# Optimization experiments

Hardware: AMD Instinct MI355X
Metric: run time of the kernel (lower is better)

Reference implementation:

```python
import jax, jax.numpy as jnp
import numpy as np

INIT_L = 512.0
EPS = 1e-6
N_HEAD = 16


def fire_bias(T, w1, b1, w2, b2, c, L_multiplier):
    # positions and relative distances
    pos = jnp.arange(T, dtype=jnp.float32)
    rel = pos[:, None] - pos[None, :]                      # (T, T)
    threshold = jnp.abs(L_multiplier * INIT_L)
    pos_norm = jnp.maximum(pos, threshold)[:, None]        # (T, 1)
    rel = jnp.log(jnp.abs(c * rel) + 1.0)                  # (T, T)
    pos_norm = jnp.log(jnp.abs(c * pos_norm) + 1.0) + EPS  # (T, 1)
    nd = rel / pos_norm                                    # (T, T)
    # tiny MLP: 1 -> mlp_width -> n_head
    h = jax.nn.relu(nd[..., None] * w1[0] + b1)            # (T, T, 32)
    bias = jnp.einsum('tsw,wh->hts', h, w2) + b2[:, None, None]  # (H, T, T)
    causal = jnp.tril(jnp.ones((T, T), dtype=bool))
    bias = jnp.where(causal[None], bias, -jnp.inf)
    return bias[None]                                      # (1, H, T, T)


def reference(x, Wqkv, bqkv, Wproj, bproj, w1, b1, w2, b2, c_param, L_multiplier):
    B, T, C = x.shape
    H = N_HEAD
    hd = C // H
    qkv = x @ Wqkv + bqkv                                  # (B, T, 3C)
    q, k, v = jnp.split(qkv, 3, axis=-1)
    q = q.reshape(B, T, H, hd).transpose(0, 2, 1, 3)       # (B, H, T, hd)
    k = k.reshape(B, T, H, hd).transpose(0, 2, 1, 3)
    v = v.reshape(B, T, H, hd).transpose(0, 2, 1, 3)
    bias = fire_bias(T, w1, b1, w2, b2, c_param, L_multiplier)  # (1, H, T, T)
    scale = 1.0 / jnp.sqrt(jnp.float32(hd))
    att = jnp.einsum('bhqd,bhkd->bhqk', q, k) * scale + bias
    att = jax.nn.softmax(att, axis=-1)
    y = jnp.einsum('bhqk,bhkd->bhqd', att, v)              # (B, H, T, hd)
    y = y.transpose(0, 2, 1, 3).reshape(B, T, C)
    return y @ Wproj + bproj


def setup_inputs() -> dict:
    key = jax.random.key(0)
    ks = jax.random.split(key, 8)
    B, T, C, H, W = 2, 2048, 1024, 16, 32
    s = 0.02
    return {
        'x': jax.random.normal(ks[0], (B, T, C), jnp.float32),
        'Wqkv': jax.random.normal(ks[1], (C, 3 * C), jnp.float32) * s,
        'bqkv': jnp.zeros((3 * C,), jnp.float32),
        'Wproj': jax.random.normal(ks[2], (C, C), jnp.float32) * s,
        'bproj': jnp.zeros((C,), jnp.float32),
        'w1': jax.random.normal(ks[3], (1, W), jnp.float32),
        'b1': jnp.zeros((W,), jnp.float32),
        'w2': jax.random.normal(ks[4], (W, H), jnp.float32) * 0.1,
        'b2': jnp.zeros((H,), jnp.float32),
        'c_param': jnp.float32(0.1),
        'L_multiplier': jnp.float32(1.0),
    }
```

## Files before the change

kernel.cpp:

```cpp
#include <hip/hip_runtime.h>
#include <cstdint>

typedef unsigned short u16;
typedef unsigned int u32;

typedef short bf16x8 __attribute__((ext_vector_type(8)));
typedef float f32x4 __attribute__((ext_vector_type(4)));

#define LN2 0.69314718055994530942f
#define LOG2E 1.44269504088896340736f
#define INFF __builtin_inff()

__device__ __forceinline__ u16 f2bf(float f) {
  u32 u = __float_as_uint(f);
  u = (u + 0x7fffu + ((u >> 16) & 1u)) >> 16;
  return (u16)u;
}
__device__ __forceinline__ u32 pack2bf(float a, float b) {
  u32 ta = __float_as_uint(a) + 0x8000u;
  u32 tb = __float_as_uint(b) + 0x8000u;
  return __builtin_amdgcn_perm(tb, ta, 0x07060302u);
}
__device__ __forceinline__ u32 pack2bf_rne(float a, float b) {
  return (u32)f2bf(a) | ((u32)f2bf(b) << 16);
}

#if __has_builtin(__builtin_amdgcn_global_load_lds)
#define HAVE_GLDS 1
__device__ __forceinline__ void glds16(const u16* g, u16* l) {
  __builtin_amdgcn_global_load_lds((const __attribute__((address_space(1))) void*)g,
                                   (__attribute__((address_space(3))) void*)l, 16, 0, 0);
}
#else
#define HAVE_GLDS 0
#endif

__device__ __forceinline__ void stage1k(const u16* gperlane, u16* lwave, int lane) {
#if HAVE_GLDS
  (void)lane;
  glds16(gperlane, lwave);
#else
  *(uint4*)(lwave + lane * 8) = *(const uint4*)gperlane;
#endif
}

__device__ __forceinline__ u16* swzp(u16* base, int row, int bc) {
  return (u16*)((char*)base + row * 128 + (bc ^ ((row & 7) << 4)));
}


__global__ void k_convert_x(const float* __restrict__ in, u16* __restrict__ out, int n4) {
  int i = blockIdx.x * blockDim.x + threadIdx.x;
  if (i < n4) {
    float4 v = ((const float4*)in)[i];
    ushort4 o;
    o.x = f2bf(v.x); o.y = f2bf(v.y); o.z = f2bf(v.z); o.w = f2bf(v.w);
    ((ushort4*)out)[i] = o;
  }
}

__global__ void k_transpose_bf(const float* __restrict__ in, u16* __restrict__ out, int R, int C) {
  __shared__ float t[32][33];
  int c0 = blockIdx.x * 32, r0 = blockIdx.y * 32;
  int tx = threadIdx.x, ty = threadIdx.y;
#pragma unroll
  for (int k = 0; k < 4; k++) t[ty + 8 * k][tx] = in[(size_t)(r0 + ty + 8 * k) * C + c0 + tx];
  __syncthreads();
#pragma unroll
  for (int k = 0; k < 4; k++) out[(size_t)(c0 + ty + 8 * k) * R + r0 + tx] = f2bf(t[tx][ty + 8 * k]);
}

__global__ void k_tables(const float* __restrict__ cP, const float* __restrict__ lP,
                         float* __restrict__ ig2, float* __restrict__ rl) {
  int t = blockIdx.x * blockDim.x + threadIdx.x;
  float c = fabsf(cP[0]);
  if (t < 2048) {
    float lm = lP[0];
    float thr = fabsf(lm * 512.0f);
    float pn = fmaxf((float)t, thr);
    float den = logf(c * pn + 1.0f) + 1e-6f;
    ig2[t] = LN2 / den;
  }
  if (t < 2112) {
    int d = t - 63;
    if (d < 0) d = 0;
    rl[t] = log2f(c * (float)d + 1.0f);
  }
}

__global__ void k_segments(const float* __restrict__ w1, const float* __restrict__ b1,
                           const float* __restrict__ w2, const float* __restrict__ b2,
                           float* __restrict__ segX, float* __restrict__ segA,
                           float* __restrict__ segB, int* __restrict__ segU) {
  __shared__ float xs[32];
  __shared__ float srt[32];
  __shared__ float uniq[32];
  __shared__ int uCnt;
  int t = threadIdx.x;
  if (t < 32) {
    float w = w1[t], b = b1[t];
    xs[t] = (w != 0.0f) ? (-b / w) : INFF;
  }
  __syncthreads();
  if (t < 32) {
    float x = xs[t];
    int r = 0;
    for (int v = 0; v < 32; v++) {
      float xv = xs[v];
      if (xv < x || (xv == x && v < t)) r++;
    }
    srt[r] = x;
  }
  __syncthreads();
  if (t == 0) {
    int u = 0;
    for (int i = 0; i < 32; i++) {
      float v = srt[i];
      if (v < 3.0e38f && (u == 0 || v != uniq[u - 1])) uniq[u++] = v;
    }
    uCnt = u;
    segU[0] = u;
  }
  __syncthreads();
  int u = uCnt;
  if (t < u) segX[t] = uniq[t];
  for (int idx = t; idx < (u + 1) * 16; idx += blockDim.x) {
    int j = idx >> 4, h = idx & 15;
    float p;
    if (u == 0) p = 0.0f;
    else if (j == 0) p = uniq[0] - 1.0f;
    else if (j == u) p = uniq[u - 1] + 1.0f;
    else p = 0.5f * (uniq[j - 1] + uniq[j]);
    float A = b2[h], B = 0.0f;
    for (int w = 0; w < 32; w++) {
      float w1w = w1[w], b1w = b1[w], w2wh = w2[w * 16 + h];
      if (w1w != 0.0f) {
        if (fmaf(w1w, p, b1w) > 0.0f) { B += w1w * w2wh; A += b1w * w2wh; }
      } else if (b1w > 0.0f) {
        A += b1w * w2wh;
      }
    }
    segA[j * 16 + h] = A;
    segB[j * 16 + h] = B;
  }
}

template <int MODE, int BN>
__launch_bounds__(256, 3)
__global__ void k_gemm(const u16* __restrict__ A, const u16* __restrict__ BT,
                       const float* __restrict__ bias, float* __restrict__ outF,
                       u16* __restrict__ outQ, u16* __restrict__ outK, u16* __restrict__ outV,
                       int M, int N, int K) {
  constexpr int NT = BN / 32;
  constexpr int NCH = BN / 32;
  __shared__ u16 As[128 * 64];
  __shared__ u16 Bs[BN * 64];
  const int tid = threadIdx.x;
  const int lane = tid & 63, wave = tid >> 6;
  const int li = lane & 15, quad = lane >> 4;
  const int wrow = (wave >> 1) * 64, wcol = (wave & 1) * (BN / 2);
  const int rb = blockIdx.y * 128, cb = blockIdx.x * BN;

  f32x4 acc[4][NT];
#pragma unroll
  for (int i = 0; i < 4; i++)
#pragma unroll
    for (int j = 0; j < NT; j++) acc[i][j] = (f32x4){0.f, 0.f, 0.f, 0.f};

#if HAVE_GLDS
  const u16* gA = A + (size_t)(rb + (tid >> 3)) * K + (tid & 7) * 8;
  const u16* gB = BT + (size_t)(cb + (tid >> 3)) * K + (tid & 7) * 8;
  u16* lA = As + wave * 512;
  u16* lB = Bs + wave * 512;

  for (int k0 = 0; k0 < K; k0 += 64) {
    __syncthreads();
#pragma unroll
    for (int ch = 0; ch < 4; ch++) glds16(gA + (size_t)ch * 32 * K + k0, lA + ch * 2048);
#pragma unroll
    for (int ch = 0; ch < NCH; ch++) glds16(gB + (size_t)ch * 32 * K + k0, lB + ch * 2048);
    __syncthreads();
#pragma unroll
    for (int c = 0; c < 2; c++) {
      bf16x8 af[4], bfr[NT];
#pragma unroll
      for (int mt = 0; mt < 4; mt++)
        af[mt] = *(const bf16x8*)(&As[(wrow + mt * 16 + li) * 64 + c * 32 + quad * 8]);
#pragma unroll
      for (int nt = 0; nt < NT; nt++)
        bfr[nt] = *(const bf16x8*)(&Bs[(wcol + nt * 16 + li) * 64 + c * 32 + quad * 8]);
#pragma unroll
      for (int mt = 0; mt < 4; mt++)
#pragma unroll
        for (int nt = 0; nt < NT; nt++)
          acc[mt][nt] = __builtin_amdgcn_mfma_f32_16x16x32_bf16(af[mt], bfr[nt], acc[mt][nt], 0, 0, 0);
    }
  }
#else
  for (int k0 = 0; k0 < K; k0 += 64) {
    __syncthreads();
    for (int idx = tid * 8; idx < 128 * 64; idx += 256 * 8) {
      int rr = idx >> 6, cc = idx & 63;
      *(uint4*)(&As[idx]) = *(const uint4*)(A + (size_t)(rb + rr) * K + k0 + cc);
    }
    for (int idx = tid * 8; idx < BN * 64; idx += 256 * 8) {
      int rr = idx >> 6, cc = idx & 63;
      *(uint4*)(&Bs[idx]) = *(const uint4*)(BT + (size_t)(cb + rr) * K + k0 + cc);
    }
    __syncthreads();
#pragma unroll
    for (int c = 0; c < 2; c++) {
      bf16x8 af[4], bfr[NT];
#pragma unroll
      for (int mt = 0; mt < 4; mt++)
        af[mt] = *(const bf16x8*)(&As[(wrow + mt * 16 + li) * 64 + c * 32 + quad * 8]);
#pragma unroll
      for (int nt = 0; nt < NT; nt++)
        bfr[nt] = *(const bf16x8*)(&Bs[(wcol + nt * 16 + li) * 64 + c * 32 + quad * 8]);
#pragma unroll
      for (int mt = 0; mt < 4; mt++)
#pragma unroll
        for (int nt = 0; nt < NT; nt++)
          acc[mt][nt] = __builtin_amdgcn_mfma_f32_16x16x32_bf16(af[mt], bfr[nt], acc[mt][nt], 0, 0, 0);
    }
  }
#endif

#pragma unroll
  for (int mt = 0; mt < 4; mt++)
#pragma unroll
    for (int nt = 0; nt < NT; nt++) {
      const int col = cb + wcol + nt * 16 + li;
      const int row0 = rb + wrow + mt * 16 + quad * 4;
      float v[4];
#pragma unroll
      for (int r = 0; r < 4; r++) v[r] = acc[mt][nt][r] + bias[col];
      if (MODE == 0) {
        const int bb = row0 >> 11, tt0 = row0 & 2047;
        const int sel = col >> 10, w = col & 1023, hh = w >> 6, dd = w & 63;
        if (sel == 0) {
          u16* dst = outQ + ((size_t)((bb * 16 + hh) * 2048 + tt0)) * 64 + dd;
#pragma unroll
          for (int r = 0; r < 4; r++) dst[(size_t)r * 64] = f2bf(v[r]);
        } else if (sel == 1) {
          u16* base = outK + ((size_t)((bb * 16 + hh) * 2048 + tt0)) * 64;
#pragma unroll
          for (int r = 0; r < 4; r++) {
            int tt = tt0 + r;
            base[(size_t)r * 64 + (dd ^ (((tt & 7)) << 3))] = f2bf(v[r]);
          }
        } else {
          u16* vrow = outV + ((size_t)((bb * 16 + hh) * 64 + dd)) * 2048;
          uint2 pk;
          pk.x = pack2bf_rne(v[0], v[1]);
          pk.y = pack2bf_rne(v[2], v[3]);
          *(uint2*)(vrow + (tt0 ^ ((dd & 7) << 3))) = pk;
        }
      } else {
#pragma unroll
        for (int r = 0; r < 4; r++) outF[(size_t)(row0 + r) * N + col] = v[r];
      }
    }
}

__launch_bounds__(256, 3)
__global__ void k_attn(const u16* __restrict__ Q, const u16* __restrict__ K,
                       const u16* __restrict__ Vt, u16* __restrict__ Y,
                       const float* __restrict__ ig2, const float* __restrict__ RL,
                       const float* __restrict__ segX, const float* __restrict__ segA,
                       const float* __restrict__ segB, const int* __restrict__ segU) {
  __shared__ u16 KsB[2 * 64 * 64];
  __shared__ u16 VtsB[2 * 64 * 64];
  __shared__ u16 Ps[64 * 64];
  __shared__ float rls[2112];
  __shared__ float sXl[32];
  __shared__ float sAl[33];
  __shared__ float sBl[33];

  const int xi = blockIdx.x, h = blockIdx.y, b = blockIdx.z;
  const int q0b = xi >> 1;
  const int flip = (xi & 1) ^ ((h >> 3) & 1);
  const int qt = flip ? (31 - q0b) : q0b;

  const int tid = threadIdx.x, lane = tid & 63, wave = tid >> 6;
  const int li = lane & 15, quad = lane >> 4;
  const int bh = b * 16 + h;
  const u16* Qg = Q + (size_t)bh * 2048 * 64;
  const u16* Kg = K + (size_t)bh * 2048 * 64;
  const u16* Vg = Vt + (size_t)bh * 64 * 2048;

  for (int i = tid; i < 2112; i += 256) rls[i] = RL[i];

  const int u = segU[0];
  float x0 = INFF, A0, B0, A1, B1;
  A0 = segA[h]; B0 = segB[h]; A1 = A0; B1 = B0;
  if (u == 1) { x0 = segX[0]; A1 = segA[16 + h]; B1 = segB[16 + h]; }
  if (u > 1) {
    if (tid < u) sXl[tid] = segX[tid];
    if (tid < u + 1) { sAl[tid] = segA[tid * 16 + h]; sBl[tid] = segB[tid * 16 + h]; }
  }
  const float A0e = A0 * LOG2E, A1e = A1 * LOG2E;
  const float SCL = 0.125f * LOG2E;

  const int t = qt * 64 + wave * 16 + li;
  bf16x8 qf[2];
#pragma unroll
  for (int c = 0; c < 2; c++)
    qf[c] = *(const bf16x8*)(Qg + (size_t)t * 64 + c * 32 + quad * 8);

  const float gI = ig2[t];
  const float x0r = x0 / gI;
  const float B0g = B0 * gI * LOG2E, B1g = B1 * gI * LOG2E;
  const bool uniB = (u <= 1) && (x0r <= 0.0f) && (A0e == A1e);
  float mrow = -INFF, lrow = 0.0f;
  f32x4 oacc[4];
#pragma unroll
  for (int nt = 0; nt < 4; nt++) oacc[nt] = (f32x4){0.f, 0.f, 0.f, 0.f};

  const u16* kgB = Kg + (size_t)(wave * 16 + (lane >> 3)) * 64 + (lane & 7) * 8;
  const u16* vgB = Vg + (size_t)(wave * 16 + (lane >> 3)) * 2048 + (lane & 7) * 8;

  auto stage = [&](int buf, int kt2) {
    u16* kd = KsB + buf * 4096 + wave * 1024;
    const u16* kg = kgB + (size_t)kt2 * 4096;
    stage1k(kg, kd, lane);
    stage1k(kg + 8 * 64, kd + 512, lane);
    u16* vd = VtsB + buf * 4096 + wave * 1024;
    const u16* vg = vgB + kt2 * 64;
    stage1k(vg, vd, lane);
    stage1k(vg + 8 * 2048, vd + 512, lane);
  };

  stage(0, 0);
  int cur = 0;

  for (int kt = 0; kt <= qt; kt++) {
    const int kb = kt * 64;
    __syncthreads();
    if (kt < qt) stage(cur ^ 1, kt + 1);

    u16* KsT = KsB + cur * 4096;
    u16* VtT = VtsB + cur * 4096;

    f32x4 sacc[4];
#pragma unroll
    for (int nt = 0; nt < 4; nt++) sacc[nt] = (f32x4){0.f, 0.f, 0.f, 0.f};
#pragma unroll
    for (int c = 0; c < 2; c++)
#pragma unroll
      for (int nt = 0; nt < 4; nt++) {
        bf16x8 kf = *(const bf16x8*)swzp(KsT, nt * 16 + li, c * 64 + quad * 16);
        sacc[nt] = __builtin_amdgcn_mfma_f32_16x16x32_bf16(kf, qf[c], sacc[nt], 0, 0, 0);
      }

    const int Cbase = t - kb - quad * 4 + 63;
    const float* rp = &rls[Cbase - 51];
    const int lim = Cbase - 63;
    if (uniB) {
#pragma unroll
      for (int nt = 0; nt < 4; nt++)
#pragma unroll
        for (int r = 0; r < 4; r++) {
          float z = fmaf(rp[51 - nt * 16 - r], B1g, sacc[nt][r] * SCL);
          if (kt == qt) z = (nt * 16 + r > lim) ? -INFF : z;
          sacc[nt][r] = z;
        }
    } else if (u <= 1) {
#pragma unroll
      for (int nt = 0; nt < 4; nt++)
#pragma unroll
        for (int r = 0; r < 4; r++) {
          float rlv = rp[51 - nt * 16 - r];
          bool hi = rlv > x0r;
          float z = fmaf(rlv, hi ? B1g : B0g, hi ? A1e : A0e);
          z = fmaf(sacc[nt][r], SCL, z);
          if (kt == qt) z = (nt * 16 + r > lim) ? -INFF : z;
          sacc[nt][r] = z;
        }
    } else {
#pragma unroll
      for (int nt = 0; nt < 4; nt++)
#pragma unroll
        for (int r = 0; r < 4; r++) {
          float nd = rp[51 - nt * 16 - r] * gI;
          int j = 0;
          for (int i = 0; i < u; i++) j += (nd > sXl[i]) ? 1 : 0;
          float z = (fmaf(nd, sBl[j], sAl[j]) + sacc[nt][r] * 0.125f) * LOG2E;
          if (kt == qt) z = (nt * 16 + r > lim) ? -INFF : z;
          sacc[nt][r] = z;
        }
    }

    f32x4 mm = sacc[0];
#pragma unroll
    for (int nt = 1; nt < 4; nt++)
#pragma unroll
      for (int r = 0; r < 4; r++) mm[r] = fmaxf(mm[r], sacc[nt][r]);
    float vm = fmaxf(fmaxf(mm[0], mm[1]), fmaxf(mm[2], mm[3]));
    vm = fmaxf(vm, __shfl_xor(vm, 16, 64));
    vm = fmaxf(vm, __shfl_xor(vm, 32, 64));
    float mnew = fmaxf(mrow, vm);
    bool grew = mnew > mrow;
    float alpha = __builtin_amdgcn_exp2f(mrow - mnew);
    mrow = mnew;
#pragma unroll
    for (int nt = 0; nt < 4; nt++)
#pragma unroll
      for (int r = 0; r < 4; r++)
        sacc[nt][r] = __builtin_amdgcn_exp2f(sacc[nt][r] - mnew);
    f32x4 sv = (sacc[0] + sacc[1]) + (sacc[2] + sacc[3]);
    float s = (sv[0] + sv[1]) + (sv[2] + sv[3]);
    s += __shfl_xor(s, 16, 64);
    s += __shfl_xor(s, 32, 64);
    lrow = lrow * alpha + s;
    if (__any(grew)) {
#pragma unroll
      for (int nt = 0; nt < 4; nt++)
#pragma unroll
        for (int r = 0; r < 4; r++) oacc[nt][r] *= alpha;
    }

    const int prow = wave * 16 + li;
#pragma unroll
    for (int nt = 0; nt < 4; nt++) {
      uint2 pk;
      pk.x = pack2bf(sacc[nt][0], sacc[nt][1]);
      pk.y = pack2bf(sacc[nt][2], sacc[nt][3]);
      *(uint2*)swzp(Ps, prow, 32 * nt + 8 * quad) = pk;
    }

#pragma unroll
    for (int c = 0; c < 2; c++) {
      bf16x8 pf = *(const bf16x8*)swzp(Ps, prow, c * 64 + quad * 16);
#pragma unroll
      for (int nt = 0; nt < 4; nt++) {
        bf16x8 vf = *(const bf16x8*)swzp(VtT, nt * 16 + li, c * 64 + quad * 16);
        oacc[nt] = __builtin_amdgcn_mfma_f32_16x16x32_bf16(vf, pf, oacc[nt], 0, 0, 0);
      }
    }
    cur ^= 1;
  }

  float inv = 1.0f / lrow;
  u16* dst = Y + (size_t)(b * 2048 + t) * 1024 + h * 64 + quad * 4;
#pragma unroll
  for (int nt = 0; nt < 4; nt++) {
    uint2 pk;
    pk.x = pack2bf(oacc[nt][0] * inv, oacc[nt][1] * inv);
    pk.y = pack2bf(oacc[nt][2] * inv, oacc[nt][3] * inv);
    *(uint2*)(dst + nt * 16) = pk;
  }
}

extern "C" void kernel_launch(void* const* d_in, const int* in_sizes, int n_in,
                              void* d_out, int out_size, void* d_ws, size_t ws_size,
                              hipStream_t stream) {
  (void)in_sizes; (void)n_in; (void)out_size; (void)ws_size;
  const float* x = (const float*)d_in[0];
  const float* Wqkv = (const float*)d_in[1];
  const float* bqkv = (const float*)d_in[2];
  const float* Wproj = (const float*)d_in[3];
  const float* bproj = (const float*)d_in[4];
  const float* w1 = (const float*)d_in[5];
  const float* b1 = (const float*)d_in[6];
  const float* w2 = (const float*)d_in[7];
  const float* b2 = (const float*)d_in[8];
  const float* cP = (const float*)d_in[9];
  const float* lP = (const float*)d_in[10];

  char* ws = (char*)d_ws;
  u16* Xbf = (u16*)(ws);
  u16* WqkvT = (u16*)(ws + (size_t)(8 << 20));
  u16* WprojT = (u16*)(ws + (size_t)(14 << 20));
  u16* Qb = (u16*)(ws + (size_t)(16 << 20));
  u16* Kb = (u16*)(ws + (size_t)(24 << 20));
  u16* Vb = (u16*)(ws + (size_t)(32 << 20));
  u16* Yb = (u16*)(ws + (size_t)(40 << 20));
  float* IG = (float*)(ws + (size_t)(48 << 20));
  float* RL = IG + 2048;
  float* SEGX = RL + 2112;
  float* SEGA = SEGX + 32;
  float* SEGB = SEGA + 33 * 16;
  int* SEGU = (int*)(SEGB + 33 * 16);

  k_convert_x<<<4096, 256, 0, stream>>>(x, Xbf, 1048576);
  k_transpose_bf<<<dim3(96, 32), dim3(32, 8), 0, stream>>>(Wqkv, WqkvT, 1024, 3072);
  k_transpose_bf<<<dim3(32, 32), dim3(32, 8), 0, stream>>>(Wproj, WprojT, 1024, 1024);
  k_tables<<<9, 256, 0, stream>>>(cP, lP, IG, RL);
  k_segments<<<1, 64, 0, stream>>>(w1, b1, w2, b2, SEGX, SEGA, SEGB, SEGU);

  k_gemm<0, 128><<<dim3(24, 32), 256, 0, stream>>>(Xbf, WqkvT, bqkv, nullptr, Qb, Kb, Vb,
                                                   4096, 3072, 1024);
  k_attn<<<dim3(32, 16, 2), 256, 0, stream>>>(Qb, Kb, Vb, Yb, IG, RL, SEGX, SEGA, SEGB, SEGU);
  k_gemm<1, 64><<<dim3(16, 32), 256, 0, stream>>>(Yb, WprojT, bproj, (float*)d_out, nullptr,
                                                  nullptr, nullptr, 4096, 1024, 1024);
}
```

Measured before the change: 239.9 us.

## Use 128-row query tiles with 8 waves, inline log bias, separate V transpose

The attention kernel now runs 512-thread blocks that cover 128 query rows, so each staged K/V tile feeds twice as many rows. The LDS log table is replaced by hardware log computed inline, and causal masking moves to a separate pass. The QKV GEMM now writes V row-major, and a new small kernel transposes and swizzles it. MFMA sections are wrapped in s_setprio hints. Together these aim to cut K/V reloads and LDS use, at the cost of an extra launch, more transcendental work per score, and worse load balance from the larger tiles.

```diff
diff --git a/kernel.cpp b/kernel.cpp
--- a/kernel.cpp
+++ b/kernel.cpp
@@ -20,9 +20,6 @@
   u32 ta = __float_as_uint(a) + 0x8000u;
   u32 tb = __float_as_uint(b) + 0x8000u;
   return __builtin_amdgcn_perm(tb, ta, 0x07060302u);
-}
-__device__ __forceinline__ u32 pack2bf_rne(float a, float b) {
-  return (u32)f2bf(a) | ((u32)f2bf(b) << 16);
 }
 
 #if __has_builtin(__builtin_amdgcn_global_load_lds)
@@ -71,7 +68,7 @@
 }
 
 __global__ void k_tables(const float* __restrict__ cP, const float* __restrict__ lP,
-                         float* __restrict__ ig2, float* __restrict__ rl) {
+                         float* __restrict__ ig2) {
   int t = blockIdx.x * blockDim.x + threadIdx.x;
   float c = fabsf(cP[0]);
   if (t < 2048) {
@@ -81,11 +78,24 @@
     float den = logf(c * pn + 1.0f) + 1e-6f;
     ig2[t] = LN2 / den;
   }
-  if (t < 2112) {
-    int d = t - 63;
-    if (d < 0) d = 0;
-    rl[t] = log2f(c * (float)d + 1.0f);
-  }
+}
+
+__global__ void k_vt(const u16* __restrict__ Vin, u16* __restrict__ Vout) {
+  __shared__ u16 ts[64][72];
+  const int tb = blockIdx.x, bh = blockIdx.y;
+  const int tid = threadIdx.x;
+  const int row = tid >> 2, c16 = (tid & 3) * 16;
+  const u16* src = Vin + (size_t)bh * 2048 * 64 + (size_t)(tb * 64 + row) * 64 + c16;
+  *(uint4*)&ts[row][c16] = *(const uint4*)src;
+  *(uint4*)&ts[row][c16 + 8] = *(const uint4*)(src + 8);
+  __syncthreads();
+  u16* drow = Vout + (size_t)bh * 64 * 2048 + (size_t)row * 2048 + tb * 64;
+  const int s = (row & 7) << 3;
+  u16 tmp[16];
+#pragma unroll
+  for (int k = 0; k < 16; k++) tmp[k] = ts[c16 + k][row];
+  *(uint4*)(drow + (c16 ^ s)) = *(uint4*)&tmp[0];
+  *(uint4*)(drow + ((c16 + 8) ^ s)) = *(uint4*)&tmp[8];
 }
 
 __global__ void k_segments(const float* __restrict__ w1, const float* __restrict__ b1,
@@ -247,14 +257,12 @@
 #pragma unroll
           for (int r = 0; r < 4; r++) {
             int tt = tt0 + r;
-            base[(size_t)r * 64 + (dd ^ (((tt & 7)) << 3))] = f2bf(v[r]);
+            base[(size_t)r * 64 + (dd ^ ((tt & 7) << 3))] = f2bf(v[r]);
           }
         } else {
-          u16* vrow = outV + ((size_t)((bb * 16 + hh) * 64 + dd)) * 2048;
-          uint2 pk;
-          pk.x = pack2bf_rne(v[0], v[1]);
-          pk.y = pack2bf_rne(v[2], v[3]);
-          *(uint2*)(vrow + (tt0 ^ ((dd & 7) << 3))) = pk;
+          u16* dst = outV + ((size_t)((bb * 16 + hh) * 2048 + tt0)) * 64 + dd;
+#pragma unroll
+          for (int r = 0; r < 4; r++) dst[(size_t)r * 64] = f2bf(v[r]);
         }
       } else {
 #pragma unroll
@@ -263,34 +271,33 @@
     }
 }
 
-__launch_bounds__(256, 3)
+__launch_bounds__(512, 4)
 __global__ void k_attn(const u16* __restrict__ Q, const u16* __restrict__ K,
                        const u16* __restrict__ Vt, u16* __restrict__ Y,
-                       const float* __restrict__ ig2, const float* __restrict__ RL,
+                       const float* __restrict__ ig2, const float* __restrict__ cP,
                        const float* __restrict__ segX, const float* __restrict__ segA,
                        const float* __restrict__ segB, const int* __restrict__ segU) {
-  __shared__ u16 KsB[2 * 64 * 64];
-  __shared__ u16 VtsB[2 * 64 * 64];
-  __shared__ u16 Ps[64 * 64];
-  __shared__ float rls[2112];
+  __shared__ u16 KsB[2 * 4096];
+  __shared__ u16 VtsB[2 * 4096];
+  __shared__ u16 Ps[128 * 64];
   __shared__ float sXl[32];
   __shared__ float sAl[33];
   __shared__ float sBl[33];
 
   const int xi = blockIdx.x, h = blockIdx.y, b = blockIdx.z;
-  const int q0b = xi >> 1;
-  const int flip = (xi & 1) ^ ((h >> 3) & 1);
-  const int qt = flip ? (31 - q0b) : q0b;
+  const int flip = (b ^ (h >> 3)) & 1;
+  const int j = flip ? (15 - xi) : xi;
+  const int ntiles = 2 * j + 2;
 
   const int tid = threadIdx.x, lane = tid & 63, wave = tid >> 6;
   const int li = lane & 15, quad = lane >> 4;
+  const int qtw = 2 * j + (wave >> 2);
   const int bh = b * 16 + h;
   const u16* Qg = Q + (size_t)bh * 2048 * 64;
   const u16* Kg = K + (size_t)bh * 2048 * 64;
   const u16* Vg = Vt + (size_t)bh * 64 * 2048;
 
-  for (int i = tid; i < 2112; i += 256) rls[i] = RL[i];
-
+  const float cAbs = fabsf(cP[0]);
   const int u = segU[0];
   float x0 = INFF, A0, B0, A1, B1;
   A0 = segA[h]; B0 = segB[h]; A1 = A0; B1 = B0;
@@ -301,8 +308,9 @@
   }
   const float A0e = A0 * LOG2E, A1e = A1 * LOG2E;
   const float SCL = 0.125f * LOG2E;
-
-  const int t = qt * 64 + wave * 16 + li;
+  const bool uniB = (u <= 1) && (x0 <= 0.0f) && (A0e == A1e);
+
+  const int t = j * 128 + wave * 16 + li;
   bf16x8 qf[2];
 #pragma unroll
   for (int c = 0; c < 2; c++)
@@ -311,33 +319,26 @@
   const float gI = ig2[t];
   const float x0r = x0 / gI;
   const float B0g = B0 * gI * LOG2E, B1g = B1 * gI * LOG2E;
-  const bool uniB = (u <= 1) && (x0r <= 0.0f) && (A0e == A1e);
   float mrow = -INFF, lrow = 0.0f;
   f32x4 oacc[4];
 #pragma unroll
   for (int nt = 0; nt < 4; nt++) oacc[nt] = (f32x4){0.f, 0.f, 0.f, 0.f};
 
-  const u16* kgB = Kg + (size_t)(wave * 16 + (lane >> 3)) * 64 + (lane & 7) * 8;
-  const u16* vgB = Vg + (size_t)(wave * 16 + (lane >> 3)) * 2048 + (lane & 7) * 8;
+  const u16* kgB = Kg + (size_t)(wave * 8 + (lane >> 3)) * 64 + (lane & 7) * 8;
+  const u16* vgB = Vg + (size_t)(wave * 8 + (lane >> 3)) * 2048 + (lane & 7) * 8;
 
   auto stage = [&](int buf, int kt2) {
-    u16* kd = KsB + buf * 4096 + wave * 1024;
-    const u16* kg = kgB + (size_t)kt2 * 4096;
-    stage1k(kg, kd, lane);
-    stage1k(kg + 8 * 64, kd + 512, lane);
-    u16* vd = VtsB + buf * 4096 + wave * 1024;
-    const u16* vg = vgB + kt2 * 64;
-    stage1k(vg, vd, lane);
-    stage1k(vg + 8 * 2048, vd + 512, lane);
+    stage1k(kgB + (size_t)kt2 * 4096, KsB + buf * 4096 + wave * 512, lane);
+    stage1k(vgB + kt2 * 64, VtsB + buf * 4096 + wave * 512, lane);
   };
 
   stage(0, 0);
   int cur = 0;
 
-  for (int kt = 0; kt <= qt; kt++) {
+  for (int kt = 0; kt < ntiles; kt++) {
     const int kb = kt * 64;
     __syncthreads();
-    if (kt < qt) stage(cur ^ 1, kt + 1);
+    if (kt + 1 < ntiles) stage(cur ^ 1, kt + 1);
 
     u16* KsT = KsB + cur * 4096;
     u16* VtT = VtsB + cur * 4096;
@@ -345,6 +346,7 @@
     f32x4 sacc[4];
 #pragma unroll
     for (int nt = 0; nt < 4; nt++) sacc[nt] = (f32x4){0.f, 0.f, 0.f, 0.f};
+    __builtin_amdgcn_s_setprio(1);
 #pragma unroll
     for (int c = 0; c < 2; c++)
 #pragma unroll
@@ -352,43 +354,47 @@
         bf16x8 kf = *(const bf16x8*)swzp(KsT, nt * 16 + li, c * 64 + quad * 16);
         sacc[nt] = __builtin_amdgcn_mfma_f32_16x16x32_bf16(kf, qf[c], sacc[nt], 0, 0, 0);
       }
-
-    const int Cbase = t - kb - quad * 4 + 63;
-    const float* rp = &rls[Cbase - 51];
-    const int lim = Cbase - 63;
+    __builtin_amdgcn_s_setprio(0);
+
+    const float dq = (float)(t - kb - quad * 4);
     if (uniB) {
 #pragma unroll
       for (int nt = 0; nt < 4; nt++)
 #pragma unroll
         for (int r = 0; r < 4; r++) {
-          float z = fmaf(rp[51 - nt * 16 - r], B1g, sacc[nt][r] * SCL);
-          if (kt == qt) z = (nt * 16 + r > lim) ? -INFF : z;
-          sacc[nt][r] = z;
+          float rl = __builtin_amdgcn_logf(fmaf(cAbs, dq - nt * 16 - r, 1.0f));
+          sacc[nt][r] = fmaf(rl, B1g, sacc[nt][r] * SCL);
         }
     } else if (u <= 1) {
 #pragma unroll
       for (int nt = 0; nt < 4; nt++)
 #pragma unroll
         for (int r = 0; r < 4; r++) {
-          float rlv = rp[51 - nt * 16 - r];
-          bool hi = rlv > x0r;
-          float z = fmaf(rlv, hi ? B1g : B0g, hi ? A1e : A0e);
-          z = fmaf(sacc[nt][r], SCL, z);
-          if (kt == qt) z = (nt * 16 + r > lim) ? -INFF : z;
-          sacc[nt][r] = z;
+          float rl = __builtin_amdgcn_logf(fmaf(cAbs, dq - nt * 16 - r, 1.0f));
+          bool hi = rl > x0r;
+          float z = fmaf(rl, hi ? B1g : B0g, hi ? A1e : A0e);
+          sacc[nt][r] = fmaf(sacc[nt][r], SCL, z);
         }
     } else {
 #pragma unroll
       for (int nt = 0; nt < 4; nt++)
 #pragma unroll
         for (int r = 0; r < 4; r++) {
-          float nd = rp[51 - nt * 16 - r] * gI;
-          int j = 0;
-          for (int i = 0; i < u; i++) j += (nd > sXl[i]) ? 1 : 0;
-          float z = (fmaf(nd, sBl[j], sAl[j]) + sacc[nt][r] * 0.125f) * LOG2E;
-          if (kt == qt) z = (nt * 16 + r > lim) ? -INFF : z;
-          sacc[nt][r] = z;
+          float rl = __builtin_amdgcn_logf(fmaf(cAbs, dq - nt * 16 - r, 1.0f));
+          float nd = rl * gI;
+          int jj = 0;
+          for (int i = 0; i < u; i++) jj += (nd > sXl[i]) ? 1 : 0;
+          sacc[nt][r] = (fmaf(nd, sBl[jj], sAl[jj]) + sacc[nt][r] * 0.125f) * LOG2E;
         }
+    }
+
+    if (kt >= qtw) {
+      const int lim = t - kb - quad * 4;
+#pragma unroll
+      for (int nt = 0; nt < 4; nt++)
+#pragma unroll
+        for (int r = 0; r < 4; r++)
+          if (nt * 16 + r > lim) sacc[nt][r] = -INFF;
     }
 
     f32x4 mm = sacc[0];
@@ -429,6 +435,7 @@
       *(uint2*)swzp(Ps, prow, 32 * nt + 8 * quad) = pk;
     }
 
+    __builtin_amdgcn_s_setprio(1);
 #pragma unroll
     for (int c = 0; c < 2; c++) {
       bf16x8 pf = *(const bf16x8*)swzp(Ps, prow, c * 64 + quad * 16);
@@ -438,6 +445,7 @@
         oacc[nt] = __builtin_amdgcn_mfma_f32_16x16x32_bf16(vf, pf, oacc[nt], 0, 0, 0);
       }
     }
+    __builtin_amdgcn_s_setprio(0);
     cur ^= 1;
   }
 
@@ -474,11 +482,11 @@
   u16* WprojT = (u16*)(ws + (size_t)(14 << 20));
   u16* Qb = (u16*)(ws + (size_t)(16 << 20));
   u16* Kb = (u16*)(ws + (size_t)(24 << 20));
-  u16* Vb = (u16*)(ws + (size_t)(32 << 20));
+  u16* Vlin = (u16*)(ws + (size_t)(32 << 20));
   u16* Yb = (u16*)(ws + (size_t)(40 << 20));
+  u16* Vtb = (u16*)(ws);
   float* IG = (float*)(ws + (size_t)(48 << 20));
-  float* RL = IG + 2048;
-  float* SEGX = RL + 2112;
+  float* SEGX = IG + 2048;
   float* SEGA = SEGX + 32;
   float* SEGB = SEGA + 33 * 16;
   int* SEGU = (int*)(SEGB + 33 * 16);
@@ -486,12 +494,13 @@
   k_convert_x<<<4096, 256, 0, stream>>>(x, Xbf, 1048576);
   k_transpose_bf<<<dim3(96, 32), dim3(32, 8), 0, stream>>>(Wqkv, WqkvT, 1024, 3072);
   k_transpose_bf<<<dim3(32, 32), dim3(32, 8), 0, stream>>>(Wproj, WprojT, 1024, 1024);
-  k_tables<<<9, 256, 0, stream>>>(cP, lP, IG, RL);
+  k_tables<<<8, 256, 0, stream>>>(cP, lP, IG);
   k_segments<<<1, 64, 0, stream>>>(w1, b1, w2, b2, SEGX, SEGA, SEGB, SEGU);
 
-  k_gemm<0, 128><<<dim3(24, 32), 256, 0, stream>>>(Xbf, WqkvT, bqkv, nullptr, Qb, Kb, Vb,
+  k_gemm<0, 128><<<dim3(24, 32), 256, 0, stream>>>(Xbf, WqkvT, bqkv, nullptr, Qb, Kb, Vlin,
                                                    4096, 3072, 1024);
-  k_attn<<<dim3(32, 16, 2), 256, 0, stream>>>(Qb, Kb, Vb, Yb, IG, RL, SEGX, SEGA, SEGB, SEGU);
+  k_vt<<<dim3(32, 32), 256, 0, stream>>>(Vlin, Vtb);
+  k_attn<<<dim3(16, 16, 2), 512, 0, stream>>>(Qb, Kb, Vtb, Yb, IG, cP, SEGX, SEGA, SEGB, SEGU);
   k_gemm<1, 64><<<dim3(16, 32), 256, 0, stream>>>(Yb, WprojT, bproj, (float*)d_out, nullptr,
                                                   nullptr, nullptr, 4096, 1024, 1024);
 }
```

After: 234.6 us. 2.2% less time.
